# Performance work log

Hardware: AMD Instinct MI355X
Metric: run time of the kernel (lower is better)

The kernel has to match this reference:

```python
import jax, jax.numpy as jnp
import numpy as np

D = 4096      # d_model
K = 8         # number of experts
L = 2048      # seq len
M = 1024      # masked positions (even indices)
U = 1024      # unmasked positions (odd indices)
DP = D // 8   # q/k projection dim = 512
H = D // 2    # expert hidden = 2048
RANGE_R = 10
PMAX = M * RANGE_R  # upper bound on number of (mask, anchor) pairs


def setup_inputs() -> dict:
    key = jax.random.key(0)
    ks = jax.random.split(key, 12)
    s = 0.02
    h_L = jax.random.normal(ks[0], (1, L, D), jnp.float32)
    # masks at even positions, unmasked at odd positions -> each mask has
    # anchors at distances 1,3,5,7,9 on each side (within range_r=10)
    mask_indices = jnp.arange(M, dtype=jnp.int32) * 2
    unmasked_indices = jnp.arange(U, dtype=jnp.int32) * 2 + 1
    Wr = jax.random.normal(ks[1], (D, K), jnp.float32) * s
    br = jnp.zeros((K,), jnp.float32)
    W1 = jax.random.normal(ks[2], (K, 2 * D, H), jnp.float32) * s
    b1 = jnp.zeros((K, H), jnp.float32)
    # NOTE: original zero-inits W2/b2 (identity router at step 0); we use random
    # init so the output is non-trivial, same math.
    W2 = jax.random.normal(ks[3], (K, H, D), jnp.float32) * s
    b2 = jnp.zeros((K, D), jnp.float32)
    Wq = jax.random.normal(ks[4], (D, DP), jnp.float32) * s
    bq = jnp.zeros((DP,), jnp.float32)
    Wk = jax.random.normal(ks[5], (D, DP), jnp.float32) * s
    bk = jnp.zeros((DP,), jnp.float32)
    return {"h_L": h_L, "mask_indices": mask_indices,
            "unmasked_indices": unmasked_indices, "range_r": RANGE_R,
            "Wr": Wr, "br": br, "W1": W1, "b1": b1, "W2": W2, "b2": b2,
            "Wq": Wq, "bq": bq, "Wk": Wk, "bk": bk}


def reference(h_L, mask_indices, unmasked_indices, range_r,
              Wr, br, W1, b1, W2, b2, Wq, bq, Wk, bk):
    h = h_L[0]                                   # [L, D] (B == 1)
    m_idx, u_idx = mask_indices, unmasked_indices
    # adjacency by distance, then static-size pair extraction
    dists = jnp.abs(m_idx[:, None] - u_idx[None, :])   # [M, U]
    adj = (dists > 0) & (dists <= range_r)
    pair_m, pair_u = jnp.nonzero(adj, size=PMAX, fill_value=-1)
    valid = pair_m >= 0
    pm = jnp.where(valid, pair_m, 0)
    pu = jnp.where(valid, pair_u, 0)
    h_masks = h[m_idx[pm]]                       # [P, D]
    h_anchors = h[u_idx[pu]]                     # [P, D]
    # routing gate over experts
    gate = jax.nn.softmax(h_masks @ Wr + br, axis=-1)  # [P, K]
    cond = jnp.concatenate([h_anchors, h_masks], axis=-1)  # [P, 2D]
    pair_deltas = jnp.zeros((PMAX, D), h.dtype)
    for e in range(K):  # fixed small expert loop
        hid = jax.nn.gelu(cond @ W1[e] + b1[e], approximate=False)
        pair_deltas = pair_deltas + gate[:, e:e + 1] * (hid @ W2[e] + b2[e])
    # q.k attention scores per pair
    q = h_masks @ Wq + bq
    k = h_anchors @ Wk + bk
    scores = (q * k).sum(-1) / (float(DP) ** 0.5)       # [P]
    scores = jnp.where(valid, scores, -1e9)
    # segment softmax over pairs grouped by mask position
    seg_max = jnp.maximum(jax.ops.segment_max(scores, pm, num_segments=M), -1e9)
    exp_s = jnp.where(valid, jnp.exp(scores - seg_max[pm]), 0.0)
    sum_exp = jax.ops.segment_sum(exp_s, pm, num_segments=M)
    combine = exp_s / jnp.maximum(sum_exp[pm], 1e-8)    # [P]
    weighted = combine[:, None] * pair_deltas           # [P, D]
    delta = jnp.zeros((L, D), h.dtype).at[m_idx[pm]].add(weighted)
    return delta[None]                                   # [1, L, D]
```

## Files before the change

kernel.cpp:

```cpp
#include <hip/hip_runtime.h>
#include <cstdint>
#include <cstddef>

#define TD 256

typedef __attribute__((ext_vector_type(8))) short short8;
typedef __attribute__((ext_vector_type(4))) float floatx4;

__device__ __forceinline__ float bf2f(short b) {
  unsigned u = ((unsigned)(unsigned short)b) << 16;
  float f;
  __builtin_memcpy(&f, &u, 4);
  return f;
}
__device__ __forceinline__ short f2bf(float f) {
  unsigned u;
  __builtin_memcpy(&u, &f, 4);
  u = u + 0x7fffu + ((u >> 16) & 1u);
  return (short)(u >> 16);
}

__device__ __forceinline__ void gload16(const void* g, void* l) {
  __builtin_amdgcn_global_load_lds(
      (const __attribute__((address_space(1))) unsigned*)g,
      (__attribute__((address_space(3))) unsigned*)l, 16, 0, 0);
}

__global__ void pack_h(const float* __restrict__ h, const int* __restrict__ midx,
                       const int* __restrict__ uidx, short* __restrict__ hm,
                       short* __restrict__ ha) {
  int r = blockIdx.x;
  int src;
  short* dst;
  if (r < 1024) { src = midx[r]; dst = hm + (size_t)r * 4096; }
  else          { src = uidx[r - 1024]; dst = ha + (size_t)(r - 1024) * 4096; }
  const float* row = h + (size_t)src * 4096;
  for (int i = threadIdx.x * 8; i < 4096; i += TD * 8) {
    float4 v0 = *(const float4*)(row + i);
    float4 v1 = *(const float4*)(row + i + 4);
    short8 o;
    o[0] = f2bf(v0.x); o[1] = f2bf(v0.y); o[2] = f2bf(v0.z); o[3] = f2bf(v0.w);
    o[4] = f2bf(v1.x); o[5] = f2bf(v1.y); o[6] = f2bf(v1.z); o[7] = f2bf(v1.w);
    *(short8*)(dst + i) = o;
  }
}

__global__ void transpose_cv(const float* __restrict__ in, int R, int C, size_t inZ,
                             short* __restrict__ out, int ldo, size_t outZ) {
  __shared__ float t[32][33];
  const float* inz = in + (size_t)blockIdx.z * inZ;
  short* outz = out + (size_t)blockIdx.z * outZ;
  int c0 = blockIdx.x * 32, r0 = blockIdx.y * 32;
  int tx = threadIdx.x & 31, ty = threadIdx.x >> 5;
#pragma unroll
  for (int i = 0; i < 4; i++)
    t[ty + i * 8][tx] = inz[(size_t)(r0 + ty + i * 8) * C + c0 + tx];
  __syncthreads();
#pragma unroll
  for (int i = 0; i < 4; i++)
    outz[(size_t)(c0 + ty + i * 8) * ldo + r0 + tx] = f2bf(t[tx][ty + i * 8]);
}

__global__ void gate_softmax(const float* __restrict__ h, const int* __restrict__ midx,
                             const float* __restrict__ Wr, const float* __restrict__ br,
                             float* __restrict__ gate) {
  int m = blockIdx.x;
  const float* row = h + (size_t)midx[m] * 4096;
  float acc[8] = {0, 0, 0, 0, 0, 0, 0, 0};
  for (int d = threadIdx.x; d < 4096; d += TD) {
    float hv = row[d];
    const float* w = Wr + (size_t)d * 8;
#pragma unroll
    for (int k = 0; k < 8; k++) acc[k] += hv * w[k];
  }
#pragma unroll
  for (int k = 0; k < 8; k++)
    for (int off = 32; off > 0; off >>= 1) acc[k] += __shfl_down(acc[k], off);
  __shared__ float red[4][8];
  int wv = threadIdx.x >> 6, lane = threadIdx.x & 63;
  if (lane == 0)
    for (int k = 0; k < 8; k++) red[wv][k] = acc[k];
  __syncthreads();
  if (threadIdx.x == 0) {
    float lg[8], mx = -3e38f;
    for (int k = 0; k < 8; k++) {
      lg[k] = red[0][k] + red[1][k] + red[2][k] + red[3][k] + br[k];
      mx = fmaxf(mx, lg[k]);
    }
    float s = 0.f;
    for (int k = 0; k < 8; k++) { lg[k] = expf(lg[k] - mx); s += lg[k]; }
    float inv = 1.f / s;
    for (int k = 0; k < 8; k++) gate[m * 8 + k] = lg[k] * inv;
  }
}

__device__ __forceinline__ void gemm_core(
    const short* __restrict__ A, const short* __restrict__ B,
    int lda, int ldb, int Kd, size_t m0, size_t n0,
    short* As, short* Bs, floatx4 (&acc)[4][4]) {
  const int tid = threadIdx.x;
  const int lane = tid & 63, wv = tid >> 6;
  const int l15 = lane & 15, quad = lane >> 4;
  const int wm = (wv >> 1) * 64, wn = (wv & 1) * 64;

#pragma unroll
  for (int i = 0; i < 4; i++)
#pragma unroll
    for (int j = 0; j < 4; j++) acc[i][j] = (floatx4){0.f, 0.f, 0.f, 0.f};

  const int c0 = tid, c1 = tid + 256;
  const short* a0g = A + (m0 + (c0 >> 2)) * (size_t)lda + (c0 & 3) * 8;
  const short* a1g = A + (m0 + (c1 >> 2)) * (size_t)lda + (c1 & 3) * 8;
  const short* b0g = B + (n0 + (c0 >> 2)) * (size_t)ldb + (c0 & 3) * 8;
  const short* b1g = B + (n0 + (c1 >> 2)) * (size_t)ldb + (c1 & 3) * 8;
  short* la0 = As + c0 * 8;
  short* la1 = As + c1 * 8;
  short* lb0 = Bs + c0 * 8;
  short* lb1 = Bs + c1 * 8;

  for (int kt = 0; kt < Kd; kt += 32) {
    gload16(a0g + kt, la0);
    gload16(a1g + kt, la1);
    gload16(b0g + kt, lb0);
    gload16(b1g + kt, lb1);
    __syncthreads();
    short8 afr[4], bfr[4];
#pragma unroll
    for (int i = 0; i < 4; i++)
      afr[i] = *(const short8*)(As + (wm + i * 16 + l15) * 32 + quad * 8);
#pragma unroll
    for (int j = 0; j < 4; j++)
      bfr[j] = *(const short8*)(Bs + (wn + j * 16 + l15) * 32 + quad * 8);
#pragma unroll
    for (int i = 0; i < 4; i++)
#pragma unroll
      for (int j = 0; j < 4; j++)
        acc[i][j] = __builtin_amdgcn_mfma_f32_16x16x32_bf16(afr[i], bfr[j], acc[i][j], 0, 0, 0);
    __syncthreads();
  }
}

__device__ __forceinline__ void epi_f32(float* __restrict__ C, int ldc, size_t m0, size_t n0,
                                        floatx4 (&acc)[4][4], const float* __restrict__ bias) {
  const int lane = threadIdx.x & 63, wv = threadIdx.x >> 6;
  const int l15 = lane & 15, quad = lane >> 4;
  const int wm = (wv >> 1) * 64, wn = (wv & 1) * 64;
  float bv[4];
#pragma unroll
  for (int j = 0; j < 4; j++) bv[j] = bias ? bias[n0 + wn + j * 16 + l15] : 0.f;
#pragma unroll
  for (int i = 0; i < 4; i++) {
#pragma unroll
    for (int r = 0; r < 4; r++) {
      size_t row = m0 + wm + i * 16 + quad * 4 + r;
      float* cp = C + row * (size_t)ldc;
#pragma unroll
      for (int j = 0; j < 4; j++)
        cp[n0 + wn + j * 16 + l15] = acc[i][j][r] + bv[j];
    }
  }
}

__device__ __forceinline__ void epi_bf16(short* __restrict__ C, int ldc, size_t m0, size_t n0,
                                         floatx4 (&acc)[4][4], const float* __restrict__ bias) {
  const int lane = threadIdx.x & 63, wv = threadIdx.x >> 6;
  const int l15 = lane & 15, quad = lane >> 4;
  const int wm = (wv >> 1) * 64, wn = (wv & 1) * 64;
  float bv[4];
#pragma unroll
  for (int j = 0; j < 4; j++) bv[j] = bias ? bias[n0 + wn + j * 16 + l15] : 0.f;
#pragma unroll
  for (int i = 0; i < 4; i++) {
#pragma unroll
    for (int r = 0; r < 4; r++) {
      size_t row = m0 + wm + i * 16 + quad * 4 + r;
      short* cp = C + row * (size_t)ldc;
#pragma unroll
      for (int j = 0; j < 4; j++)
        cp[n0 + wn + j * 16 + l15] = f2bf(acc[i][j][r] + bv[j]);
    }
  }
}

__global__ __launch_bounds__(256) void gemm_qk(
    const short* __restrict__ hm, const short* __restrict__ ha,
    const short* __restrict__ WqT, const short* __restrict__ WkT,
    const float* __restrict__ bq, const float* __restrict__ bk,
    float* __restrict__ qb, float* __restrict__ kb) {
  __shared__ __align__(16) short As[128 * 32];
  __shared__ __align__(16) short Bs[128 * 32];
  const short* A = blockIdx.z ? ha : hm;
  const short* B = blockIdx.z ? WkT : WqT;
  const float* bias = blockIdx.z ? bk : bq;
  float* C = blockIdx.z ? kb : qb;
  size_t m0 = (size_t)blockIdx.y * 128, n0 = (size_t)blockIdx.x * 128;
  floatx4 acc[4][4];
  gemm_core(A, B, 4096, 4096, 4096, m0, n0, As, Bs, acc);
  epi_f32(C, 512, m0, n0, acc, bias);
}

__global__ __launch_bounds__(256) void gemm_w1(
    const short* __restrict__ ha, const short* __restrict__ hm,
    const short* __restrict__ W1T, const float* __restrict__ b1,
    short* __restrict__ A1, short* __restrict__ M1) {
  __shared__ __align__(16) short As[128 * 32];
  __shared__ __align__(16) short Bs[128 * 32];
  const int z = blockIdx.z, e = z >> 1, half = z & 1;
  const short* A = half ? hm : ha;
  const short* B = W1T + (size_t)e * 2048 * 8192 + (size_t)half * 4096;
  const float* bias = half ? (b1 + (size_t)e * 2048) : nullptr;
  short* C = (half ? M1 : A1) + (size_t)e * 1024 * 2048;
  size_t m0 = (size_t)blockIdx.y * 128, n0 = (size_t)blockIdx.x * 128;
  floatx4 acc[4][4];
  gemm_core(A, B, 4096, 8192, 4096, m0, n0, As, Bs, acc);
  epi_bf16(C, 2048, m0, n0, acc, bias);
}

__global__ __launch_bounds__(256) void gemm_w2(
    const short* __restrict__ Gp, const short* __restrict__ W2T,
    float* __restrict__ deltaP) {
  __shared__ __align__(16) short As[128 * 32];
  __shared__ __align__(16) short Bs[128 * 32];
  const int z = blockIdx.z;
  const short* A = Gp + (size_t)z * 4096;
  const short* B = W2T + (size_t)z * 4096;
  float* C = deltaP + (size_t)z * 1024 * 4096;
  size_t m0 = (size_t)blockIdx.y * 128, n0 = (size_t)blockIdx.x * 128;
  floatx4 acc[4][4];
  gemm_core(A, B, 16384, 16384, 4096, m0, n0, As, Bs, acc);
  epi_f32(C, 4096, m0, n0, acc, nullptr);
}

__global__ void scores_combine(const float* __restrict__ qb, const float* __restrict__ kb,
                               float* __restrict__ comb) {
  int m = blockIdx.x;
  int lane = threadIdx.x;
  float qr[8];
#pragma unroll
  for (int i = 0; i < 8; i++) qr[i] = qb[(size_t)m * 512 + i * 64 + lane];
  float sc[10];
  for (int s = 0; s < 10; s++) {
    int u = m - 5 + s;
    float val = -3e38f;
    if (u >= 0 && u < 1024) {
      const float* kr = kb + (size_t)u * 512;
      float p = 0.f;
#pragma unroll
      for (int i = 0; i < 8; i++) p += qr[i] * kr[i * 64 + lane];
      for (int off = 32; off > 0; off >>= 1) p += __shfl_down(p, off);
      val = p * 0.04419417382415922f;
    }
    sc[s] = val;
  }
  if (lane == 0) {
    float mx = -3e38f;
    for (int s = 0; s < 10; s++) mx = fmaxf(mx, sc[s]);
    float e[10], sum = 0.f;
    for (int s = 0; s < 10; s++) {
      e[s] = (sc[s] > -1e38f) ? expf(sc[s] - mx) : 0.f;
      sum += e[s];
    }
    float inv = 1.f / fmaxf(sum, 1e-8f);
    for (int s = 0; s < 10; s++) comb[m * 10 + s] = e[s] * inv;
  }
}

__global__ void reduce_G(const short* __restrict__ A1, const short* __restrict__ M1,
                         const float* __restrict__ comb, const float* __restrict__ gate,
                         short* __restrict__ Gp) {
  int m = blockIdx.x, e = blockIdx.y;
  int h0 = threadIdx.x * 8;
  short8 mv = *(const short8*)(M1 + ((size_t)e * 1024 + m) * 2048 + h0);
  float m1v[8];
#pragma unroll
  for (int i = 0; i < 8; i++) m1v[i] = bf2f(mv[i]);
  float acc[8] = {0, 0, 0, 0, 0, 0, 0, 0};
  float g = gate[m * 8 + e];
#pragma unroll
  for (int s = 0; s < 10; s++) {
    int u = m - 5 + s;
    if (u < 0 || u >= 1024) continue;
    float c = comb[m * 10 + s];
    short8 av = *(const short8*)(A1 + ((size_t)e * 1024 + u) * 2048 + h0);
#pragma unroll
    for (int i = 0; i < 8; i++) {
      float x = bf2f(av[i]) + m1v[i];
      float gl = 0.5f * x * (1.f + erff(x * 0.7071067811865475f));
      acc[i] += c * gl;
    }
  }
  short8 o;
#pragma unroll
  for (int i = 0; i < 8; i++) o[i] = f2bf(g * acc[i]);
  *(short8*)(Gp + (size_t)m * 16384 + e * 2048 + h0) = o;
}

__global__ void scatter_out(const float* __restrict__ deltaP, const float* __restrict__ gate,
                            const float* __restrict__ b2, const int* __restrict__ midx,
                            float* __restrict__ out) {
  int m = blockIdx.x;
  float g[8];
#pragma unroll
  for (int e = 0; e < 8; e++) g[e] = gate[m * 8 + e];
  const float* dr = deltaP + (size_t)m * 4096;
  const size_t zs = (size_t)1024 * 4096;
  float* orow = out + (size_t)midx[m] * 4096;
  for (int d = threadIdx.x * 4; d < 4096; d += TD * 4) {
    float4 v = *(const float4*)(dr + d);
    float4 v1 = *(const float4*)(dr + zs + d);
    float4 v2 = *(const float4*)(dr + 2 * zs + d);
    float4 v3 = *(const float4*)(dr + 3 * zs + d);
    v.x += v1.x + v2.x + v3.x; v.y += v1.y + v2.y + v3.y;
    v.z += v1.z + v2.z + v3.z; v.w += v1.w + v2.w + v3.w;
#pragma unroll
    for (int e = 0; e < 8; e++) {
      float4 b = *(const float4*)(b2 + (size_t)e * 4096 + d);
      v.x += g[e] * b.x; v.y += g[e] * b.y; v.z += g[e] * b.z; v.w += g[e] * b.w;
    }
    *(float4*)(orow + d) = v;
  }
}

extern "C" void kernel_launch(void* const* d_in, const int* in_sizes, int n_in,
                              void* d_out, int out_size, void* d_ws, size_t ws_size,
                              hipStream_t stream) {
  const float* h   = (const float*)d_in[0];
  const int* midx  = (const int*)d_in[1];
  const int* uidx  = (const int*)d_in[2];
  const float* Wr  = (const float*)d_in[4];
  const float* br  = (const float*)d_in[5];
  const float* W1  = (const float*)d_in[6];
  const float* b1  = (const float*)d_in[7];
  const float* W2  = (const float*)d_in[8];
  const float* b2  = (const float*)d_in[9];
  const float* Wq  = (const float*)d_in[10];
  const float* bq  = (const float*)d_in[11];
  const float* Wk  = (const float*)d_in[12];
  const float* bk  = (const float*)d_in[13];
  float* out = (float*)d_out;

  char* p = (char*)d_ws;
  short* hm   = (short*)p; p += (size_t)1024 * 4096 * 2;
  short* ha   = (short*)p; p += (size_t)1024 * 4096 * 2;
  short* WqT  = (short*)p; p += (size_t)512 * 4096 * 2;
  short* WkT  = (short*)p; p += (size_t)512 * 4096 * 2;
  float* qb   = (float*)p; p += (size_t)1024 * 512 * 4;
  float* kb   = (float*)p; p += (size_t)1024 * 512 * 4;
  float* gate = (float*)p; p += (size_t)1024 * 8 * 4;
  float* comb = (float*)p; p += (size_t)1024 * 16 * 4;
  short* W1T  = (short*)p; p += (size_t)8 * 2048 * 8192 * 2;
  short* A1   = (short*)p; p += (size_t)8 * 1024 * 2048 * 2;
  short* M1   = (short*)p; p += (size_t)8 * 1024 * 2048 * 2;
  short* Gp   = (short*)p; p += (size_t)1024 * 16384 * 2;
  short* W2T  = (short*)p; p += (size_t)4096 * 16384 * 2;
  float* deltaP = (float*)p; p += (size_t)4 * 1024 * 4096 * 4;

  hipMemsetAsync(out, 0, (size_t)out_size * sizeof(float), stream);
  pack_h<<<2048, TD, 0, stream>>>(h, midx, uidx, hm, ha);
  gate_softmax<<<1024, TD, 0, stream>>>(h, midx, Wr, br, gate);

  transpose_cv<<<dim3(16, 128, 1), TD, 0, stream>>>(Wq, 4096, 512, 0, WqT, 4096, 0);
  transpose_cv<<<dim3(16, 128, 1), TD, 0, stream>>>(Wk, 4096, 512, 0, WkT, 4096, 0);
  gemm_qk<<<dim3(4, 8, 2), TD, 0, stream>>>(hm, ha, WqT, WkT, bq, bk, qb, kb);
  scores_combine<<<1024, 64, 0, stream>>>(qb, kb, comb);

  transpose_cv<<<dim3(64, 256, 8), TD, 0, stream>>>(
      W1, 8192, 2048, (size_t)8192 * 2048, W1T, 8192, (size_t)2048 * 8192);
  gemm_w1<<<dim3(16, 8, 16), TD, 0, stream>>>(ha, hm, W1T, b1, A1, M1);

  reduce_G<<<dim3(1024, 8), TD, 0, stream>>>(A1, M1, comb, gate, Gp);

  transpose_cv<<<dim3(128, 64, 8), TD, 0, stream>>>(
      W2, 2048, 4096, (size_t)2048 * 4096, W2T, 16384, 2048);
  gemm_w2<<<dim3(32, 8, 4), TD, 0, stream>>>(Gp, W2T, deltaP);

  scatter_out<<<1024, TD, 0, stream>>>(deltaP, gate, b2, midx, out);
}
```

Measured before the change: 1.800 ms.

## Vectorize weight transposes, split-K the q/k GEMM, and use fast GELU approximation

The transpose kernel moves to 64x64 tiles with float4 loads and 8-wide bf16 stores, which cuts memory transactions when converting the large W1/W2 weights every call. The q/k projection GEMM is split into four K-chunks so the small 1024x512 problem launches more blocks, and the partial sums plus biases are added in scores_combine. The GELU in reduce_G swaps erff for an Abramowitz-Stegun polynomial with __expf, which is cheaper but less accurate. Extra partial buffers and redundant k-row partial reads add some memory traffic.

```diff
diff --git a/kernel.cpp b/kernel.cpp
--- a/kernel.cpp
+++ b/kernel.cpp
@@ -24,6 +24,19 @@
   __builtin_amdgcn_global_load_lds(
       (const __attribute__((address_space(1))) unsigned*)g,
       (__attribute__((address_space(3))) unsigned*)l, 16, 0, 0);
+}
+
+__device__ __forceinline__ float gelu_exact(float x) {
+  float ax = fabsf(x) * 0.7071067811865475f;
+  float t = 1.f / fmaf(0.3275911f, ax, 1.f);
+  float poly = t * (0.254829592f +
+               t * (-0.284496736f +
+               t * (1.421413741f +
+               t * (-1.453152027f +
+               t * 1.061405429f))));
+  float erfv = 1.f - poly * __expf(-ax * ax);
+  erfv = copysignf(erfv, x);
+  return 0.5f * x * (1.f + erfv);
 }
 
 __global__ void pack_h(const float* __restrict__ h, const int* __restrict__ midx,
@@ -47,18 +60,31 @@
 
 __global__ void transpose_cv(const float* __restrict__ in, int R, int C, size_t inZ,
                              short* __restrict__ out, int ldo, size_t outZ) {
-  __shared__ float t[32][33];
+  __shared__ float t[64][65];
   const float* inz = in + (size_t)blockIdx.z * inZ;
   short* outz = out + (size_t)blockIdx.z * outZ;
-  int c0 = blockIdx.x * 32, r0 = blockIdx.y * 32;
-  int tx = threadIdx.x & 31, ty = threadIdx.x >> 5;
-#pragma unroll
-  for (int i = 0; i < 4; i++)
-    t[ty + i * 8][tx] = inz[(size_t)(r0 + ty + i * 8) * C + c0 + tx];
+  int c0 = blockIdx.x * 64, r0 = blockIdx.y * 64;
+  int lr = threadIdx.x >> 4;
+  int lc4 = (threadIdx.x & 15) * 4;
+#pragma unroll
+  for (int i = 0; i < 4; i++) {
+    float4 v = *(const float4*)(inz + (size_t)(r0 + lr + i * 16) * C + c0 + lc4);
+    t[lr + i * 16][lc4 + 0] = v.x;
+    t[lr + i * 16][lc4 + 1] = v.y;
+    t[lr + i * 16][lc4 + 2] = v.z;
+    t[lr + i * 16][lc4 + 3] = v.w;
+  }
   __syncthreads();
-#pragma unroll
-  for (int i = 0; i < 4; i++)
-    outz[(size_t)(c0 + ty + i * 8) * ldo + r0 + tx] = f2bf(t[tx][ty + i * 8]);
+  int oc = threadIdx.x >> 3;
+  int or8 = (threadIdx.x & 7) * 8;
+#pragma unroll
+  for (int p = 0; p < 2; p++) {
+    int c = oc + p * 32;
+    short8 o;
+#pragma unroll
+    for (int q = 0; q < 8; q++) o[q] = f2bf(t[or8 + q][c]);
+    *(short8*)(outz + (size_t)(c0 + c) * ldo + r0 + or8) = o;
+  }
 }
 
 __global__ void gate_softmax(const float* __restrict__ h, const int* __restrict__ midx,
@@ -185,18 +211,17 @@
 __global__ __launch_bounds__(256) void gemm_qk(
     const short* __restrict__ hm, const short* __restrict__ ha,
     const short* __restrict__ WqT, const short* __restrict__ WkT,
-    const float* __restrict__ bq, const float* __restrict__ bk,
-    float* __restrict__ qb, float* __restrict__ kb) {
+    float* __restrict__ qbP, float* __restrict__ kbP) {
   __shared__ __align__(16) short As[128 * 32];
   __shared__ __align__(16) short Bs[128 * 32];
-  const short* A = blockIdx.z ? ha : hm;
-  const short* B = blockIdx.z ? WkT : WqT;
-  const float* bias = blockIdx.z ? bk : bq;
-  float* C = blockIdx.z ? kb : qb;
+  const int isK = blockIdx.z & 1, kc = blockIdx.z >> 1;
+  const short* A = (isK ? ha : hm) + kc * 1024;
+  const short* B = (isK ? WkT : WqT) + kc * 1024;
+  float* C = (isK ? kbP : qbP) + (size_t)kc * 1024 * 512;
   size_t m0 = (size_t)blockIdx.y * 128, n0 = (size_t)blockIdx.x * 128;
   floatx4 acc[4][4];
-  gemm_core(A, B, 4096, 4096, 4096, m0, n0, As, Bs, acc);
-  epi_f32(C, 512, m0, n0, acc, bias);
+  gemm_core(A, B, 4096, 4096, 1024, m0, n0, As, Bs, acc);
+  epi_f32(C, 512, m0, n0, acc, nullptr);
 }
 
 __global__ __launch_bounds__(256) void gemm_w1(
@@ -231,22 +256,32 @@
   epi_f32(C, 4096, m0, n0, acc, nullptr);
 }
 
-__global__ void scores_combine(const float* __restrict__ qb, const float* __restrict__ kb,
+__global__ void scores_combine(const float* __restrict__ qbP, const float* __restrict__ kbP,
+                               const float* __restrict__ bq, const float* __restrict__ bk,
                                float* __restrict__ comb) {
   int m = blockIdx.x;
   int lane = threadIdx.x;
+  const size_t ZS = (size_t)1024 * 512;
   float qr[8];
 #pragma unroll
-  for (int i = 0; i < 8; i++) qr[i] = qb[(size_t)m * 512 + i * 64 + lane];
+  for (int i = 0; i < 8; i++) {
+    int d = i * 64 + lane;
+    const float* q0 = qbP + (size_t)m * 512 + d;
+    qr[i] = bq[d] + q0[0] + q0[ZS] + q0[2 * ZS] + q0[3 * ZS];
+  }
   float sc[10];
   for (int s = 0; s < 10; s++) {
     int u = m - 5 + s;
     float val = -3e38f;
     if (u >= 0 && u < 1024) {
-      const float* kr = kb + (size_t)u * 512;
+      const float* k0 = kbP + (size_t)u * 512;
       float p = 0.f;
 #pragma unroll
-      for (int i = 0; i < 8; i++) p += qr[i] * kr[i * 64 + lane];
+      for (int i = 0; i < 8; i++) {
+        int d = i * 64 + lane;
+        float kv = bk[d] + k0[d] + k0[ZS + d] + k0[2 * ZS + d] + k0[3 * ZS + d];
+        p += qr[i] * kv;
+      }
       for (int off = 32; off > 0; off >>= 1) p += __shfl_down(p, off);
       val = p * 0.04419417382415922f;
     }
@@ -285,8 +320,7 @@
 #pragma unroll
     for (int i = 0; i < 8; i++) {
       float x = bf2f(av[i]) + m1v[i];
-      float gl = 0.5f * x * (1.f + erff(x * 0.7071067811865475f));
-      acc[i] += c * gl;
+      acc[i] += c * gelu_exact(x);
     }
   }
   short8 o;
@@ -344,8 +378,8 @@
   short* ha   = (short*)p; p += (size_t)1024 * 4096 * 2;
   short* WqT  = (short*)p; p += (size_t)512 * 4096 * 2;
   short* WkT  = (short*)p; p += (size_t)512 * 4096 * 2;
-  float* qb   = (float*)p; p += (size_t)1024 * 512 * 4;
-  float* kb   = (float*)p; p += (size_t)1024 * 512 * 4;
+  float* qbP  = (float*)p; p += (size_t)4 * 1024 * 512 * 4;
+  float* kbP  = (float*)p; p += (size_t)4 * 1024 * 512 * 4;
   float* gate = (float*)p; p += (size_t)1024 * 8 * 4;
   float* comb = (float*)p; p += (size_t)1024 * 16 * 4;
   short* W1T  = (short*)p; p += (size_t)8 * 2048 * 8192 * 2;
@@ -359,18 +393,18 @@
   pack_h<<<2048, TD, 0, stream>>>(h, midx, uidx, hm, ha);
   gate_softmax<<<1024, TD, 0, stream>>>(h, midx, Wr, br, gate);
 
-  transpose_cv<<<dim3(16, 128, 1), TD, 0, stream>>>(Wq, 4096, 512, 0, WqT, 4096, 0);
-  transpose_cv<<<dim3(16, 128, 1), TD, 0, stream>>>(Wk, 4096, 512, 0, WkT, 4096, 0);
-  gemm_qk<<<dim3(4, 8, 2), TD, 0, stream>>>(hm, ha, WqT, WkT, bq, bk, qb, kb);
-  scores_combine<<<1024, 64, 0, stream>>>(qb, kb, comb);
-
-  transpose_cv<<<dim3(64, 256, 8), TD, 0, stream>>>(
+  transpose_cv<<<dim3(8, 64, 1), TD, 0, stream>>>(Wq, 4096, 512, 0, WqT, 4096, 0);
+  transpose_cv<<<dim3(8, 64, 1), TD, 0, stream>>>(Wk, 4096, 512, 0, WkT, 4096, 0);
+  gemm_qk<<<dim3(4, 8, 8), TD, 0, stream>>>(hm, ha, WqT, WkT, qbP, kbP);
+  scores_combine<<<1024, 64, 0, stream>>>(qbP, kbP, bq, bk, comb);
+
+  transpose_cv<<<dim3(32, 128, 8), TD, 0, stream>>>(
       W1, 8192, 2048, (size_t)8192 * 2048, W1T, 8192, (size_t)2048 * 8192);
   gemm_w1<<<dim3(16, 8, 16), TD, 0, stream>>>(ha, hm, W1T, b1, A1, M1);
 
   reduce_G<<<dim3(1024, 8), TD, 0, stream>>>(A1, M1, comb, gate, Gp);
 
-  transpose_cv<<<dim3(128, 64, 8), TD, 0, stream>>>(
+  transpose_cv<<<dim3(64, 32, 8), TD, 0, stream>>>(
       W2, 2048, 4096, (size_t)2048 * 4096, W2T, 16384, 2048);
   gemm_w2<<<dim3(32, 8, 4), TD, 0, stream>>>(Gp, W2T, deltaP);
 
```

New measurement: 1.725 ms. 1.04x faster.
